# Kernel optimization log

Hardware: AMD Instinct MI355X
Metric: run time of the kernel (lower is better)

The kernel has to match this reference:

```python
import jax, jax.numpy as jnp
import numpy as np

N_NODES = 50000
N_EDGES = 800000
D_FEAT = 64
UNITS = 64


def setup_inputs() -> dict:
    key = jax.random.key(0)
    k1, k2, k3, k4, k5 = jax.random.split(key, 5)
    embeddings = jax.random.normal(k1, (N_NODES, D_FEAT), dtype=jnp.float32)
    edge_src = jax.random.randint(k2, (N_EDGES,), 0, N_NODES, dtype=jnp.int32)
    edge_dst = jax.random.randint(k3, (N_EDGES,), 0, N_NODES, dtype=jnp.int32)
    # normalized-adjacency-like positive weights
    edge_w = jax.random.uniform(k4, (N_EDGES,), dtype=jnp.float32)
    # keras 'truncated_normal' initializer default stddev=0.05 (approx w/ normal)
    kernel = jax.random.normal(k5, (D_FEAT, UNITS), dtype=jnp.float32) * 0.05
    return {"embeddings": embeddings, "edge_src": edge_src,
            "edge_dst": edge_dst, "edge_w": edge_w, "kernel": kernel}


def reference(embeddings, edge_src, edge_dst, edge_w, kernel):
    # SpMM: agg[i] = sum_{e: dst(e)=i} w_e * embeddings[src(e)]
    msgs = embeddings[edge_src] * edge_w[:, None]            # [E, D]
    agg = jax.ops.segment_sum(msgs, edge_dst,
                              num_segments=embeddings.shape[0])  # [N, D]
    # dense GEMM + relu (use_bias=False)
    return jax.nn.relu(agg @ kernel)                          # [N, units]
```

## Files before the change

### kernel.cpp

```cpp
#include <hip/hip_runtime.h>
#include <hip/hip_bf16.h>

#define D    64
#define CH   4096
#define BKT  32
#define PASS 1024

__global__ __launch_bounds__(256) void gemm_part(
    const float* __restrict__ emb,
    const float* __restrict__ W,
    __hip_bfloat16* __restrict__ Zb,
    const int*   __restrict__ dst,
    int*         __restrict__ histG,
    ushort*      __restrict__ lrank,
    int N, int E, int NB, int gemmTiles)
{
    __shared__ int smem[4096];

    if ((int)blockIdx.x >= gemmTiles) {
        const int c  = (int)blockIdx.x - gemmTiles;
        const int t  = threadIdx.x;
        for (int b = t; b < NB; b += 256) smem[b] = 0;
        __syncthreads();
        const int e0 = c * CH;
#pragma unroll
        for (int i = 0; i < 16; ++i) {
            int e = e0 + i * 256 + t;
            if (e < E) {
                int b = dst[e] / BKT;
                lrank[e] = (ushort)atomicAdd(&smem[b], 1);
            }
        }
        __syncthreads();
        for (int b = t; b < NB; b += 256)
            histG[(size_t)c * NB + b] = smem[b];
        return;
    }

    const int lane = threadIdx.x & 63;
    const int wave = threadIdx.x >> 6;

    float wcol[D];
#pragma unroll
    for (int k = 0; k < D; ++k) wcol[k] = W[k * D + lane];

    float* At = (float*)smem;
    const int row0 = blockIdx.x * 64;

    for (int i = threadIdx.x; i < 1024; i += 256) {
        int r  = i >> 4;
        int gr = row0 + r;
        float4 v;
        if (gr < N) v = reinterpret_cast<const float4*>(emb)[(size_t)gr * 16 + (i & 15)];
        else        v = float4{0.f, 0.f, 0.f, 0.f};
        reinterpret_cast<float4*>(At)[i] = v;
    }
    __syncthreads();

    for (int rr = 0; rr < 16; ++rr) {
        int r  = wave * 16 + rr;
        int gr = row0 + r;
        if (gr >= N) break;
        const float4* arow = reinterpret_cast<const float4*>(At + r * D);
        float acc = 0.f;
#pragma unroll
        for (int k4 = 0; k4 < 16; ++k4) {
            float4 a = arow[k4];
            acc = fmaf(a.x, wcol[4 * k4 + 0], acc);
            acc = fmaf(a.y, wcol[4 * k4 + 1], acc);
            acc = fmaf(a.z, wcol[4 * k4 + 2], acc);
            acc = fmaf(a.w, wcol[4 * k4 + 3], acc);
        }
        Zb[(size_t)gr * D + lane] = __float2bfloat16(acc);
    }
}

__global__ __launch_bounds__(256) void scan_hist(
    const int* __restrict__ histG, int* __restrict__ offsets,
    int* __restrict__ partials, int NB, int NC, int M)
{
    __shared__ int sh[256];
    const int t    = threadIdx.x;
    const int base = blockIdx.x * 4096 + t * 16;

    int v[16], ps[16];
    int b = base / NC, c = base - b * NC;
#pragma unroll
    for (int k = 0; k < 16; ++k) {
        int m = base + k;
        v[k] = (m < M) ? histG[(size_t)c * NB + b] : 0;
        if (++c == NC) { c = 0; ++b; }
    }
    int s = 0;
#pragma unroll
    for (int k = 0; k < 16; ++k) { ps[k] = s; s += v[k]; }
    sh[t] = s;
    __syncthreads();
    for (int off = 1; off < 256; off <<= 1) {
        int x = (t >= off) ? sh[t - off] : 0;
        __syncthreads();
        sh[t] += x;
        __syncthreads();
    }
    const int excl = sh[t] - s;
#pragma unroll
    for (int k = 0; k < 4; ++k) {
        int4 o;
        o.x = excl + ps[4*k+0]; o.y = excl + ps[4*k+1];
        o.z = excl + ps[4*k+2]; o.w = excl + ps[4*k+3];
        reinterpret_cast<int4*>(offsets + base)[k] = o;
    }
    if (t == 255) partials[blockIdx.x] = sh[255];
}

__device__ __forceinline__ void scan_partials_lds256(
    const int* __restrict__ partials, int nb, int* sp)
{
    const int t    = threadIdx.x;
    const int orig = (t < nb) ? partials[t] : 0;
    sp[t] = orig;
    __syncthreads();
    for (int off = 1; off < 256; off <<= 1) {
        int x = (t >= off) ? sp[t - off] : 0;
        __syncthreads();
        sp[t] += x;
        __syncthreads();
    }
    int incl = sp[t];
    __syncthreads();
    sp[t] = incl - orig;
    __syncthreads();
}

__global__ __launch_bounds__(256) void scatter_bkt(
    const int*    __restrict__ src,
    const int*    __restrict__ dst,
    const float*  __restrict__ w,
    const ushort* __restrict__ lrank,
    const int*    __restrict__ histG,
    const int*    __restrict__ offsets,
    const int*    __restrict__ partials,
    int2*         __restrict__ csr,
    int E, int NB, int NC, int nb2)
{
    __shared__ int2   rec[CH];
    __shared__ ushort bidv[CH];
    __shared__ int    delta[1568];
    __shared__ int    sh[256];
    __shared__ int    sp[256];
    scan_partials_lds256(partials, nb2, sp);

    const int t  = threadIdx.x;
    const int c  = blockIdx.x;
    const int e0 = c * CH;
    const int cnt = min(CH, E - e0);

    int hv[7], hps[7];
    const int hbase = t * 7;
#pragma unroll
    for (int k = 0; k < 7; ++k) {
        int b = hbase + k;
        hv[k] = (b < NB) ? histG[(size_t)c * NB + b] : 0;
    }
    int s = 0;
#pragma unroll
    for (int k = 0; k < 7; ++k) { hps[k] = s; s += hv[k]; }
    sh[t] = s;
    __syncthreads();
    for (int off = 1; off < 256; off <<= 1) {
        int x = (t >= off) ? sh[t - off] : 0;
        __syncthreads();
        sh[t] += x;
        __syncthreads();
    }
    const int hexcl = sh[t] - s;
#pragma unroll
    for (int k = 0; k < 7; ++k) {
        int b = hbase + k;
        if (b < NB) delta[b] = hexcl + hps[k];
    }
    __syncthreads();

#pragma unroll
    for (int i = 0; i < 16; ++i) {
        int e = e0 + i * 256 + t;
        if (e < E) {
            int d  = dst[e];
            int b  = d / BKT;
            int lp = delta[b] + lrank[e];
            rec[lp]  = make_int2(src[e] | ((d & (BKT - 1)) << 16), __float_as_int(w[e]));
            bidv[lp] = (ushort)b;
        }
    }
    __syncthreads();

#pragma unroll
    for (int k = 0; k < 7; ++k) {
        int b = hbase + k;
        if (b < NB) {
            int m = b * NC + c;
            delta[b] = offsets[m] + sp[m >> 12] - delta[b];
        }
    }
    __syncthreads();

    for (int j = t; j < cnt; j += 256)
        csr[j + delta[bidv[j]]] = rec[j];
}

__global__ __launch_bounds__(256) void aggregate(
    const __hip_bfloat16* __restrict__ Zb,
    const int2* __restrict__ csr,
    const int*  __restrict__ offsets,
    const int*  __restrict__ partials,
    float*      __restrict__ out,
    int N, int E, int NB, int NC, int nb2)
{
    __shared__ int2 srec[PASS];
    __shared__ int  hist[BKT];
    __shared__ int  nbase[BKT + 1];
    __shared__ int  sp[256];
    scan_partials_lds256(partials, nb2, sp);

    const int t = threadIdx.x;
    const int b = blockIdx.x;

    const int m0 = b * NC;
    const int bStart = offsets[m0] + sp[m0 >> 12];
    int bEnd;
    if (b + 1 < NB) { int m1 = (b + 1) * NC; bEnd = offsets[m1] + sp[m1 >> 12]; }
    else            bEnd = E;

    const int wv   = t >> 6;
    const int lane = t & 63;
    const int slot = lane >> 3;
    const int q    = lane & 7;

    const int4* Zq = reinterpret_cast<const int4*>(Zb);

    float4 alo[8], ahi[8];
#pragma unroll
    for (int r = 0; r < 8; ++r) { alo[r] = float4{0,0,0,0}; ahi[r] = float4{0,0,0,0}; }

    for (int cur = bStart; cur < bEnd; cur += PASS) {
        const int cnt = min(PASS, bEnd - cur);

        if (t < BKT) hist[t] = 0;
        __syncthreads();

        int2 myrec[4]; int mypos[4];
#pragma unroll
        for (int k = 0; k < 4; ++k) {
            int j = k * 256 + t;
            if (j < cnt) {
                int2 r2 = csr[cur + j];
                myrec[k] = r2;
                mypos[k] = atomicAdd(&hist[(r2.x >> 16) & (BKT - 1)], 1);
            }
        }
        __syncthreads();

        if (t < BKT) {
            int v = hist[t];
            int x = v;
            for (int off = 1; off < BKT; off <<= 1) {
                int y = __shfl_up(x, off, 64);
                if (t >= off) x += y;
            }
            nbase[t] = x - v;
            if (t == BKT - 1) nbase[BKT] = x;
        }
        __syncthreads();

#pragma unroll
        for (int k = 0; k < 4; ++k) {
            int j = k * 256 + t;
            if (j < cnt)
                srec[nbase[(myrec[k].x >> 16) & (BKT - 1)] + mypos[k]] = myrec[k];
        }
        __syncthreads();

        for (int r = 0; r < 8; ++r) {
            const int nl = wv * 8 + r;
            const int je = nbase[nl + 1];
            for (int j = nbase[nl] + slot; j < je; j += 8) {
                int2  e  = srec[j];
                float ww = __int_as_float(e.y);
                int   sn = e.x & 0xFFFF;
                int4  zz = Zq[(size_t)sn * 8 + q];
                alo[r].x = fmaf(ww, __uint_as_float((unsigned)zz.x << 16),          alo[r].x);
                alo[r].y = fmaf(ww, __uint_as_float((unsigned)zz.x & 0xFFFF0000u),  alo[r].y);
                alo[r].z = fmaf(ww, __uint_as_float((unsigned)zz.y << 16),          alo[r].z);
                alo[r].w = fmaf(ww, __uint_as_float((unsigned)zz.y & 0xFFFF0000u),  alo[r].w);
                ahi[r].x = fmaf(ww, __uint_as_float((unsigned)zz.z << 16),          ahi[r].x);
                ahi[r].y = fmaf(ww, __uint_as_float((unsigned)zz.z & 0xFFFF0000u),  ahi[r].y);
                ahi[r].z = fmaf(ww, __uint_as_float((unsigned)zz.w << 16),          ahi[r].z);
                ahi[r].w = fmaf(ww, __uint_as_float((unsigned)zz.w & 0xFFFF0000u),  ahi[r].w);
            }
        }
        __syncthreads();
    }

    const int node0 = b * BKT + wv * 8;
#pragma unroll
    for (int r = 0; r < 8; ++r) {
        float4 lo = alo[r], hi = ahi[r];
#pragma unroll
        for (int off = 32; off >= 8; off >>= 1) {
            lo.x += __shfl_down(lo.x, off, 64);
            lo.y += __shfl_down(lo.y, off, 64);
            lo.z += __shfl_down(lo.z, off, 64);
            lo.w += __shfl_down(lo.w, off, 64);
            hi.x += __shfl_down(hi.x, off, 64);
            hi.y += __shfl_down(hi.y, off, 64);
            hi.z += __shfl_down(hi.z, off, 64);
            hi.w += __shfl_down(hi.w, off, 64);
        }
        int node = node0 + r;
        if (lane < 8 && node < N) {
            float4 o0, o1;
            o0.x = fmaxf(lo.x, 0.f); o0.y = fmaxf(lo.y, 0.f);
            o0.z = fmaxf(lo.z, 0.f); o0.w = fmaxf(lo.w, 0.f);
            o1.x = fmaxf(hi.x, 0.f); o1.y = fmaxf(hi.y, 0.f);
            o1.z = fmaxf(hi.z, 0.f); o1.w = fmaxf(hi.w, 0.f);
            float4* orow = reinterpret_cast<float4*>(out) + (size_t)node * 16 + lane * 2;
            orow[0] = o0;
            orow[1] = o1;
        }
    }
}

extern "C" void kernel_launch(void* const* d_in, const int* in_sizes, int n_in,
                              void* d_out, int out_size, void* d_ws, size_t ws_size,
                              hipStream_t stream)
{
    const float* emb  = (const float*)d_in[0];
    const int*   esrc = (const int*)  d_in[1];
    const int*   edst = (const int*)  d_in[2];
    const float* ew   = (const float*)d_in[3];
    const float* W    = (const float*)d_in[4];
    float*       out  = (float*)d_out;

    const int N  = in_sizes[0] / D;
    const int E  = in_sizes[1];

    const int NB  = (N + BKT - 1) / BKT;
    const int NC  = (E + CH - 1) / CH;
    const int M   = NB * NC;
    const int nb2 = (M + 4095) / 4096;
    const int Mpad = nb2 * 4096;

    char* p = (char*)d_ws;
    __hip_bfloat16* Zb = (__hip_bfloat16*)p;  p += (size_t)N * D * 2;
    int*    histG   = (int*)p;                p += (size_t)Mpad * 4;
    int*    offsets = (int*)p;                p += (size_t)Mpad * 4;
    int*    partials= (int*)p;                p += 256 * 4;
    ushort* lrank   = (ushort*)p;             p += (size_t)((E + 7) & ~7) * 2;
    int2*   csr     = (int2*)p;

    const int gemmTiles = (N + 63) / 64;
    gemm_part<<<gemmTiles + NC, 256, 0, stream>>>(
        emb, W, Zb, edst, histG, lrank, N, E, NB, gemmTiles);

    scan_hist<<<nb2, 256, 0, stream>>>(histG, offsets, partials, NB, NC, M);

    scatter_bkt<<<NC, 256, 0, stream>>>(
        esrc, edst, ew, lrank, histG, offsets, partials, csr, E, NB, NC, nb2);

    aggregate<<<NB, 256, 0, stream>>>(
        Zb, csr, offsets, partials, out, N, E, NB, NC, nb2);
}
```

Baseline: 147.4 us.

## Fuse all four stages into one cooperative persistent kernel with grid syncs

Replaces the four separate launches (GEMM+histogram, scan, scatter, aggregate) with one persistent cooperative kernel that uses grid-wide syncs between phases. The histogram is now stored bucket-major so the scan reads it contiguously. The scatter phase recomputes each chunk's local histogram rather than reading it back. This is meant to remove launch gaps and redundant per-block partial scans, at the cost of grid.sync overhead, a grid capped at occupancy-based persistent size, and a 48KB shared buffer that may limit occupancy.

```diff
diff --git a/kernel.cpp b/kernel.cpp
--- a/kernel.cpp
+++ b/kernel.cpp
@@ -1,331 +1,296 @@
 #include <hip/hip_runtime.h>
+#include <hip/hip_cooperative_groups.h>
 #include <hip/hip_bf16.h>
+
+namespace cg = cooperative_groups;
 
 #define D    64
 #define CH   4096
 #define BKT  32
 #define PASS 1024
-
-__global__ __launch_bounds__(256) void gemm_part(
+#define SU   2048
+
+__global__ __launch_bounds__(256, 2) void fused(
     const float* __restrict__ emb,
     const float* __restrict__ W,
+    const int*   __restrict__ esrc,
+    const int*   __restrict__ edst,
+    const float* __restrict__ ew,
+    float*       __restrict__ out,
     __hip_bfloat16* __restrict__ Zb,
-    const int*   __restrict__ dst,
-    int*         __restrict__ histG,
-    ushort*      __restrict__ lrank,
-    int N, int E, int NB, int gemmTiles)
+    int*    __restrict__ histG,
+    int*    __restrict__ offsets,
+    int*    __restrict__ partials,
+    ushort* __restrict__ lrank,
+    int2*   __restrict__ csr,
+    int N, int E, int NB, int NC, int M, int units, int gemmTiles)
 {
-    __shared__ int smem[4096];
-
-    if ((int)blockIdx.x >= gemmTiles) {
-        const int c  = (int)blockIdx.x - gemmTiles;
-        const int t  = threadIdx.x;
-        for (int b = t; b < NB; b += 256) smem[b] = 0;
+    __shared__ __align__(16) char smem[49152];
+    cg::grid_group grid = cg::this_grid();
+    const int t = threadIdx.x;
+    const int G = gridDim.x;
+
+    for (int it = blockIdx.x; it < gemmTiles + NC; it += G) {
         __syncthreads();
-        const int e0 = c * CH;
-#pragma unroll
-        for (int i = 0; i < 16; ++i) {
-            int e = e0 + i * 256 + t;
-            if (e < E) {
-                int b = dst[e] / BKT;
-                lrank[e] = (ushort)atomicAdd(&smem[b], 1);
-            }
-        }
+        if (it < gemmTiles) {
+            float* At = (float*)smem;
+            const int lane = t & 63, wave = t >> 6;
+            float wcol[D];
+#pragma unroll
+            for (int k = 0; k < D; ++k) wcol[k] = W[k * D + lane];
+            const int row0 = it * 64;
+            for (int i = t; i < 1024; i += 256) {
+                int r = i >> 4, gr = row0 + r;
+                float4 v = (gr < N)
+                    ? reinterpret_cast<const float4*>(emb)[(size_t)gr * 16 + (i & 15)]
+                    : float4{0.f, 0.f, 0.f, 0.f};
+                reinterpret_cast<float4*>(At)[i] = v;
+            }
+            __syncthreads();
+            for (int rr = 0; rr < 16; ++rr) {
+                int r = wave * 16 + rr, gr = row0 + r;
+                if (gr >= N) break;
+                const float4* arow = reinterpret_cast<const float4*>(At + r * D);
+                float acc = 0.f;
+#pragma unroll
+                for (int k4 = 0; k4 < 16; ++k4) {
+                    float4 a = arow[k4];
+                    acc = fmaf(a.x, wcol[4 * k4 + 0], acc);
+                    acc = fmaf(a.y, wcol[4 * k4 + 1], acc);
+                    acc = fmaf(a.z, wcol[4 * k4 + 2], acc);
+                    acc = fmaf(a.w, wcol[4 * k4 + 3], acc);
+                }
+                Zb[(size_t)gr * D + lane] = __float2bfloat16(acc);
+            }
+        } else {
+            const int c = it - gemmTiles;
+            int* hist = (int*)smem;
+            for (int b = t; b < NB; b += 256) hist[b] = 0;
+            __syncthreads();
+            const int e0 = c * CH;
+#pragma unroll
+            for (int i = 0; i < 16; ++i) {
+                int e = e0 + i * 256 + t;
+                if (e < E)
+                    lrank[e] = (ushort)atomicAdd(&hist[edst[e] >> 5], 1);
+            }
+            __syncthreads();
+            for (int b = t; b < NB; b += 256)
+                histG[(size_t)b * NC + c] = hist[b];
+        }
+    }
+    grid.sync();
+
+    for (int u = blockIdx.x; u < units; u += G) {
         __syncthreads();
-        for (int b = t; b < NB; b += 256)
-            histG[(size_t)c * NB + b] = smem[b];
-        return;
-    }
-
-    const int lane = threadIdx.x & 63;
-    const int wave = threadIdx.x >> 6;
-
-    float wcol[D];
-#pragma unroll
-    for (int k = 0; k < D; ++k) wcol[k] = W[k * D + lane];
-
-    float* At = (float*)smem;
-    const int row0 = blockIdx.x * 64;
-
-    for (int i = threadIdx.x; i < 1024; i += 256) {
-        int r  = i >> 4;
-        int gr = row0 + r;
-        float4 v;
-        if (gr < N) v = reinterpret_cast<const float4*>(emb)[(size_t)gr * 16 + (i & 15)];
-        else        v = float4{0.f, 0.f, 0.f, 0.f};
-        reinterpret_cast<float4*>(At)[i] = v;
-    }
-    __syncthreads();
-
-    for (int rr = 0; rr < 16; ++rr) {
-        int r  = wave * 16 + rr;
-        int gr = row0 + r;
-        if (gr >= N) break;
-        const float4* arow = reinterpret_cast<const float4*>(At + r * D);
-        float acc = 0.f;
-#pragma unroll
-        for (int k4 = 0; k4 < 16; ++k4) {
-            float4 a = arow[k4];
-            acc = fmaf(a.x, wcol[4 * k4 + 0], acc);
-            acc = fmaf(a.y, wcol[4 * k4 + 1], acc);
-            acc = fmaf(a.z, wcol[4 * k4 + 2], acc);
-            acc = fmaf(a.w, wcol[4 * k4 + 3], acc);
-        }
-        Zb[(size_t)gr * D + lane] = __float2bfloat16(acc);
-    }
-}
-
-__global__ __launch_bounds__(256) void scan_hist(
-    const int* __restrict__ histG, int* __restrict__ offsets,
-    int* __restrict__ partials, int NB, int NC, int M)
-{
-    __shared__ int sh[256];
-    const int t    = threadIdx.x;
-    const int base = blockIdx.x * 4096 + t * 16;
-
-    int v[16], ps[16];
-    int b = base / NC, c = base - b * NC;
-#pragma unroll
-    for (int k = 0; k < 16; ++k) {
-        int m = base + k;
-        v[k] = (m < M) ? histG[(size_t)c * NB + b] : 0;
-        if (++c == NC) { c = 0; ++b; }
-    }
-    int s = 0;
-#pragma unroll
-    for (int k = 0; k < 16; ++k) { ps[k] = s; s += v[k]; }
-    sh[t] = s;
-    __syncthreads();
-    for (int off = 1; off < 256; off <<= 1) {
-        int x = (t >= off) ? sh[t - off] : 0;
+        int* sh = (int*)smem;
+        const int base = u * SU + t * 8;
+        int v[8], ps[8];
+#pragma unroll
+        for (int k = 0; k < 8; ++k) {
+            int m = base + k;
+            v[k] = (m < M) ? histG[m] : 0;
+        }
+        int s = 0;
+#pragma unroll
+        for (int k = 0; k < 8; ++k) { ps[k] = s; s += v[k]; }
+        sh[t] = s;
         __syncthreads();
-        sh[t] += x;
+        for (int off = 1; off < 256; off <<= 1) {
+            int x = (t >= off) ? sh[t - off] : 0;
+            __syncthreads();
+            sh[t] += x;
+            __syncthreads();
+        }
+        const int excl = sh[t] - s;
+#pragma unroll
+        for (int k = 0; k < 8; ++k)
+            offsets[base + k] = excl + ps[k];
+        if (t == 255) partials[u] = sh[255];
+    }
+    grid.sync();
+
+    if (blockIdx.x == 0) {
+        int* sh = (int*)smem;
+        int orig = (t < units) ? partials[t] : 0;
+        sh[t] = orig;
         __syncthreads();
-    }
-    const int excl = sh[t] - s;
-#pragma unroll
-    for (int k = 0; k < 4; ++k) {
-        int4 o;
-        o.x = excl + ps[4*k+0]; o.y = excl + ps[4*k+1];
-        o.z = excl + ps[4*k+2]; o.w = excl + ps[4*k+3];
-        reinterpret_cast<int4*>(offsets + base)[k] = o;
-    }
-    if (t == 255) partials[blockIdx.x] = sh[255];
-}
-
-__device__ __forceinline__ void scan_partials_lds256(
-    const int* __restrict__ partials, int nb, int* sp)
-{
-    const int t    = threadIdx.x;
-    const int orig = (t < nb) ? partials[t] : 0;
-    sp[t] = orig;
-    __syncthreads();
-    for (int off = 1; off < 256; off <<= 1) {
-        int x = (t >= off) ? sp[t - off] : 0;
-        __syncthreads();
-        sp[t] += x;
-        __syncthreads();
-    }
-    int incl = sp[t];
-    __syncthreads();
-    sp[t] = incl - orig;
-    __syncthreads();
-}
-
-__global__ __launch_bounds__(256) void scatter_bkt(
-    const int*    __restrict__ src,
-    const int*    __restrict__ dst,
-    const float*  __restrict__ w,
-    const ushort* __restrict__ lrank,
-    const int*    __restrict__ histG,
-    const int*    __restrict__ offsets,
-    const int*    __restrict__ partials,
-    int2*         __restrict__ csr,
-    int E, int NB, int NC, int nb2)
-{
-    __shared__ int2   rec[CH];
-    __shared__ ushort bidv[CH];
-    __shared__ int    delta[1568];
-    __shared__ int    sh[256];
-    __shared__ int    sp[256];
-    scan_partials_lds256(partials, nb2, sp);
-
-    const int t  = threadIdx.x;
-    const int c  = blockIdx.x;
-    const int e0 = c * CH;
-    const int cnt = min(CH, E - e0);
-
-    int hv[7], hps[7];
-    const int hbase = t * 7;
-#pragma unroll
-    for (int k = 0; k < 7; ++k) {
-        int b = hbase + k;
-        hv[k] = (b < NB) ? histG[(size_t)c * NB + b] : 0;
-    }
-    int s = 0;
-#pragma unroll
-    for (int k = 0; k < 7; ++k) { hps[k] = s; s += hv[k]; }
-    sh[t] = s;
-    __syncthreads();
-    for (int off = 1; off < 256; off <<= 1) {
-        int x = (t >= off) ? sh[t - off] : 0;
-        __syncthreads();
-        sh[t] += x;
-        __syncthreads();
-    }
-    const int hexcl = sh[t] - s;
-#pragma unroll
-    for (int k = 0; k < 7; ++k) {
-        int b = hbase + k;
-        if (b < NB) delta[b] = hexcl + hps[k];
-    }
-    __syncthreads();
-
-#pragma unroll
-    for (int i = 0; i < 16; ++i) {
-        int e = e0 + i * 256 + t;
-        if (e < E) {
-            int d  = dst[e];
-            int b  = d / BKT;
-            int lp = delta[b] + lrank[e];
-            rec[lp]  = make_int2(src[e] | ((d & (BKT - 1)) << 16), __float_as_int(w[e]));
-            bidv[lp] = (ushort)b;
-        }
-    }
-    __syncthreads();
-
-#pragma unroll
-    for (int k = 0; k < 7; ++k) {
-        int b = hbase + k;
-        if (b < NB) {
-            int m = b * NC + c;
-            delta[b] = offsets[m] + sp[m >> 12] - delta[b];
-        }
-    }
-    __syncthreads();
-
-    for (int j = t; j < cnt; j += 256)
-        csr[j + delta[bidv[j]]] = rec[j];
-}
-
-__global__ __launch_bounds__(256) void aggregate(
-    const __hip_bfloat16* __restrict__ Zb,
-    const int2* __restrict__ csr,
-    const int*  __restrict__ offsets,
-    const int*  __restrict__ partials,
-    float*      __restrict__ out,
-    int N, int E, int NB, int NC, int nb2)
-{
-    __shared__ int2 srec[PASS];
-    __shared__ int  hist[BKT];
-    __shared__ int  nbase[BKT + 1];
-    __shared__ int  sp[256];
-    scan_partials_lds256(partials, nb2, sp);
-
-    const int t = threadIdx.x;
-    const int b = blockIdx.x;
-
-    const int m0 = b * NC;
-    const int bStart = offsets[m0] + sp[m0 >> 12];
-    int bEnd;
-    if (b + 1 < NB) { int m1 = (b + 1) * NC; bEnd = offsets[m1] + sp[m1 >> 12]; }
-    else            bEnd = E;
-
-    const int wv   = t >> 6;
-    const int lane = t & 63;
-    const int slot = lane >> 3;
-    const int q    = lane & 7;
-
-    const int4* Zq = reinterpret_cast<const int4*>(Zb);
-
-    float4 alo[8], ahi[8];
-#pragma unroll
-    for (int r = 0; r < 8; ++r) { alo[r] = float4{0,0,0,0}; ahi[r] = float4{0,0,0,0}; }
-
-    for (int cur = bStart; cur < bEnd; cur += PASS) {
-        const int cnt = min(PASS, bEnd - cur);
-
-        if (t < BKT) hist[t] = 0;
-        __syncthreads();
-
-        int2 myrec[4]; int mypos[4];
-#pragma unroll
-        for (int k = 0; k < 4; ++k) {
-            int j = k * 256 + t;
-            if (j < cnt) {
-                int2 r2 = csr[cur + j];
-                myrec[k] = r2;
-                mypos[k] = atomicAdd(&hist[(r2.x >> 16) & (BKT - 1)], 1);
-            }
-        }
-        __syncthreads();
-
-        if (t < BKT) {
-            int v = hist[t];
-            int x = v;
-            for (int off = 1; off < BKT; off <<= 1) {
-                int y = __shfl_up(x, off, 64);
-                if (t >= off) x += y;
-            }
-            nbase[t] = x - v;
-            if (t == BKT - 1) nbase[BKT] = x;
-        }
-        __syncthreads();
-
-#pragma unroll
-        for (int k = 0; k < 4; ++k) {
-            int j = k * 256 + t;
-            if (j < cnt)
-                srec[nbase[(myrec[k].x >> 16) & (BKT - 1)] + mypos[k]] = myrec[k];
-        }
-        __syncthreads();
-
-        for (int r = 0; r < 8; ++r) {
-            const int nl = wv * 8 + r;
-            const int je = nbase[nl + 1];
-            for (int j = nbase[nl] + slot; j < je; j += 8) {
-                int2  e  = srec[j];
-                float ww = __int_as_float(e.y);
-                int   sn = e.x & 0xFFFF;
-                int4  zz = Zq[(size_t)sn * 8 + q];
-                alo[r].x = fmaf(ww, __uint_as_float((unsigned)zz.x << 16),          alo[r].x);
-                alo[r].y = fmaf(ww, __uint_as_float((unsigned)zz.x & 0xFFFF0000u),  alo[r].y);
-                alo[r].z = fmaf(ww, __uint_as_float((unsigned)zz.y << 16),          alo[r].z);
-                alo[r].w = fmaf(ww, __uint_as_float((unsigned)zz.y & 0xFFFF0000u),  alo[r].w);
-                ahi[r].x = fmaf(ww, __uint_as_float((unsigned)zz.z << 16),          ahi[r].x);
-                ahi[r].y = fmaf(ww, __uint_as_float((unsigned)zz.z & 0xFFFF0000u),  ahi[r].y);
-                ahi[r].z = fmaf(ww, __uint_as_float((unsigned)zz.w << 16),          ahi[r].z);
-                ahi[r].w = fmaf(ww, __uint_as_float((unsigned)zz.w & 0xFFFF0000u),  ahi[r].w);
-            }
-        }
-        __syncthreads();
-    }
-
-    const int node0 = b * BKT + wv * 8;
-#pragma unroll
-    for (int r = 0; r < 8; ++r) {
-        float4 lo = alo[r], hi = ahi[r];
-#pragma unroll
-        for (int off = 32; off >= 8; off >>= 1) {
-            lo.x += __shfl_down(lo.x, off, 64);
-            lo.y += __shfl_down(lo.y, off, 64);
-            lo.z += __shfl_down(lo.z, off, 64);
-            lo.w += __shfl_down(lo.w, off, 64);
-            hi.x += __shfl_down(hi.x, off, 64);
-            hi.y += __shfl_down(hi.y, off, 64);
-            hi.z += __shfl_down(hi.z, off, 64);
-            hi.w += __shfl_down(hi.w, off, 64);
-        }
-        int node = node0 + r;
-        if (lane < 8 && node < N) {
-            float4 o0, o1;
-            o0.x = fmaxf(lo.x, 0.f); o0.y = fmaxf(lo.y, 0.f);
-            o0.z = fmaxf(lo.z, 0.f); o0.w = fmaxf(lo.w, 0.f);
-            o1.x = fmaxf(hi.x, 0.f); o1.y = fmaxf(hi.y, 0.f);
-            o1.z = fmaxf(hi.z, 0.f); o1.w = fmaxf(hi.w, 0.f);
-            float4* orow = reinterpret_cast<float4*>(out) + (size_t)node * 16 + lane * 2;
-            orow[0] = o0;
-            orow[1] = o1;
+        for (int off = 1; off < 256; off <<= 1) {
+            int x = (t >= off) ? sh[t - off] : 0;
+            __syncthreads();
+            sh[t] += x;
+            __syncthreads();
+        }
+        if (t < units) partials[t] = sh[t] - orig;
+    }
+    grid.sync();
+
+    {
+        int2*   rec  = (int2*)smem;
+        ushort* bidv = (ushort*)(smem + 32768);
+        int*    lcnt = (int*)(smem + 40960);
+        int*    sh   = (int*)(smem + 47232);
+        for (int c = blockIdx.x; c < NC; c += G) {
+            __syncthreads();
+            const int e0  = c * CH;
+            const int cnt = min(CH, E - e0);
+            for (int b = t; b < NB; b += 256) lcnt[b] = 0;
+            __syncthreads();
+#pragma unroll
+            for (int i = 0; i < 16; ++i) {
+                int e = e0 + i * 256 + t;
+                if (e < E) atomicAdd(&lcnt[edst[e] >> 5], 1);
+            }
+            __syncthreads();
+            int hv[7], ps[7];
+            const int hbase = t * 7;
+#pragma unroll
+            for (int k = 0; k < 7; ++k) {
+                int b = hbase + k;
+                hv[k] = (b < NB) ? lcnt[b] : 0;
+            }
+            int s = 0;
+#pragma unroll
+            for (int k = 0; k < 7; ++k) { ps[k] = s; s += hv[k]; }
+            sh[t] = s;
+            __syncthreads();
+            for (int off = 1; off < 256; off <<= 1) {
+                int x = (t >= off) ? sh[t - off] : 0;
+                __syncthreads();
+                sh[t] += x;
+                __syncthreads();
+            }
+            const int hexcl = sh[t] - s;
+#pragma unroll
+            for (int k = 0; k < 7; ++k) {
+                int b = hbase + k;
+                if (b < NB) lcnt[b] = hexcl + ps[k];
+            }
+            __syncthreads();
+#pragma unroll
+            for (int i = 0; i < 16; ++i) {
+                int e = e0 + i * 256 + t;
+                if (e < E) {
+                    int d  = edst[e];
+                    int b  = d >> 5;
+                    int lp = lcnt[b] + lrank[e];
+                    rec[lp]  = make_int2(esrc[e] | ((d & 31) << 16), __float_as_int(ew[e]));
+                    bidv[lp] = (ushort)b;
+                }
+            }
+            __syncthreads();
+#pragma unroll
+            for (int k = 0; k < 7; ++k) {
+                int b = hbase + k;
+                if (b < NB) {
+                    int m = b * NC + c;
+                    lcnt[b] = offsets[m] + partials[m >> 11] - lcnt[b];
+                }
+            }
+            __syncthreads();
+            for (int j = t; j < cnt; j += 256)
+                csr[j + lcnt[bidv[j]]] = rec[j];
+        }
+    }
+    grid.sync();
+
+    {
+        int2* srec  = (int2*)smem;
+        int*  hist  = (int*)(smem + 8192);
+        int*  nbase = (int*)(smem + 8192 + 128);
+        const int wv = t >> 6, lane = t & 63, slot = lane >> 3, q = lane & 7;
+        const int4* Zq = reinterpret_cast<const int4*>(Zb);
+
+        for (int b = blockIdx.x; b < NB; b += G) {
+            __syncthreads();
+            const int m0 = b * NC, m1 = m0 + NC;
+            const int bStart = offsets[m0] + partials[m0 >> 11];
+            const int bEnd   = offsets[m1] + partials[m1 >> 11];
+
+            float4 alo[8], ahi[8];
+#pragma unroll
+            for (int r = 0; r < 8; ++r) { alo[r] = float4{0,0,0,0}; ahi[r] = float4{0,0,0,0}; }
+
+            for (int cur = bStart; cur < bEnd; cur += PASS) {
+                const int cnt = min(PASS, bEnd - cur);
+                if (t < BKT) hist[t] = 0;
+                __syncthreads();
+                int2 myrec[4]; int mypos[4];
+#pragma unroll
+                for (int k = 0; k < 4; ++k) {
+                    int j = k * 256 + t;
+                    if (j < cnt) {
+                        int2 r2 = csr[cur + j];
+                        myrec[k] = r2;
+                        mypos[k] = atomicAdd(&hist[(r2.x >> 16) & (BKT - 1)], 1);
+                    }
+                }
+                __syncthreads();
+                if (t < BKT) {
+                    int v = hist[t], x = v;
+                    for (int off = 1; off < BKT; off <<= 1) {
+                        int y = __shfl_up(x, off, 64);
+                        if (t >= off) x += y;
+                    }
+                    nbase[t] = x - v;
+                    if (t == BKT - 1) nbase[BKT] = x;
+                }
+                __syncthreads();
+#pragma unroll
+                for (int k = 0; k < 4; ++k) {
+                    int j = k * 256 + t;
+                    if (j < cnt)
+                        srec[nbase[(myrec[k].x >> 16) & (BKT - 1)] + mypos[k]] = myrec[k];
+                }
+                __syncthreads();
+                for (int r = 0; r < 8; ++r) {
+                    const int nl = wv * 8 + r;
+                    const int je = nbase[nl + 1];
+                    for (int j = nbase[nl] + slot; j < je; j += 8) {
+                        int2  e  = srec[j];
+                        float ww = __int_as_float(e.y);
+                        int   sn = e.x & 0xFFFF;
+                        int4  zz = Zq[(size_t)sn * 8 + q];
+                        alo[r].x = fmaf(ww, __uint_as_float((unsigned)zz.x << 16),         alo[r].x);
+                        alo[r].y = fmaf(ww, __uint_as_float((unsigned)zz.x & 0xFFFF0000u), alo[r].y);
+                        alo[r].z = fmaf(ww, __uint_as_float((unsigned)zz.y << 16),         alo[r].z);
+                        alo[r].w = fmaf(ww, __uint_as_float((unsigned)zz.y & 0xFFFF0000u), alo[r].w);
+                        ahi[r].x = fmaf(ww, __uint_as_float((unsigned)zz.z << 16),         ahi[r].x);
+                        ahi[r].y = fmaf(ww, __uint_as_float((unsigned)zz.z & 0xFFFF0000u), ahi[r].y);
+                        ahi[r].z = fmaf(ww, __uint_as_float((unsigned)zz.w << 16),         ahi[r].z);
+                        ahi[r].w = fmaf(ww, __uint_as_float((unsigned)zz.w & 0xFFFF0000u), ahi[r].w);
+                    }
+                }
+                __syncthreads();
+            }
+
+            const int node0 = b * BKT + wv * 8;
+#pragma unroll
+            for (int r = 0; r < 8; ++r) {
+                float4 lo = alo[r], hi = ahi[r];
+#pragma unroll
+                for (int off = 32; off >= 8; off >>= 1) {
+                    lo.x += __shfl_down(lo.x, off, 64);
+                    lo.y += __shfl_down(lo.y, off, 64);
+                    lo.z += __shfl_down(lo.z, off, 64);
+                    lo.w += __shfl_down(lo.w, off, 64);
+                    hi.x += __shfl_down(hi.x, off, 64);
+                    hi.y += __shfl_down(hi.y, off, 64);
+                    hi.z += __shfl_down(hi.z, off, 64);
+                    hi.w += __shfl_down(hi.w, off, 64);
+                }
+                int node = node0 + r;
+                if (lane < 8 && node < N) {
+                    float4 o0, o1;
+                    o0.x = fmaxf(lo.x, 0.f); o0.y = fmaxf(lo.y, 0.f);
+                    o0.z = fmaxf(lo.z, 0.f); o0.w = fmaxf(lo.w, 0.f);
+                    o1.x = fmaxf(hi.x, 0.f); o1.y = fmaxf(hi.y, 0.f);
+                    o1.z = fmaxf(hi.z, 0.f); o1.w = fmaxf(hi.w, 0.f);
+                    float4* orow = reinterpret_cast<float4*>(out) + (size_t)node * 16 + lane * 2;
+                    orow[0] = o0;
+                    orow[1] = o1;
+                }
+            }
         }
     }
 }
@@ -344,29 +309,32 @@
     const int N  = in_sizes[0] / D;
     const int E  = in_sizes[1];
 
-    const int NB  = (N + BKT - 1) / BKT;
-    const int NC  = (E + CH - 1) / CH;
-    const int M   = NB * NC;
-    const int nb2 = (M + 4095) / 4096;
-    const int Mpad = nb2 * 4096;
+    const int NB    = (N + BKT - 1) / BKT;
+    const int NC    = (E + CH - 1) / CH;
+    const int M     = NB * NC;
+    const int units = (M + SU - 1) / SU;
+    const int Mpad  = units * SU;
+    const int gemmTiles = (N + 63) / 64;
 
     char* p = (char*)d_ws;
     __hip_bfloat16* Zb = (__hip_bfloat16*)p;  p += (size_t)N * D * 2;
-    int*    histG   = (int*)p;                p += (size_t)Mpad * 4;
-    int*    offsets = (int*)p;                p += (size_t)Mpad * 4;
-    int*    partials= (int*)p;                p += 256 * 4;
-    ushort* lrank   = (ushort*)p;             p += (size_t)((E + 7) & ~7) * 2;
-    int2*   csr     = (int2*)p;
-
-    const int gemmTiles = (N + 63) / 64;
-    gemm_part<<<gemmTiles + NC, 256, 0, stream>>>(
-        emb, W, Zb, edst, histG, lrank, N, E, NB, gemmTiles);
-
-    scan_hist<<<nb2, 256, 0, stream>>>(histG, offsets, partials, NB, NC, M);
-
-    scatter_bkt<<<NC, 256, 0, stream>>>(
-        esrc, edst, ew, lrank, histG, offsets, partials, csr, E, NB, NC, nb2);
-
-    aggregate<<<NB, 256, 0, stream>>>(
-        Zb, csr, offsets, partials, out, N, E, NB, NC, nb2);
+    int*    histG    = (int*)p;               p += (size_t)Mpad * 4;
+    int*    offsets  = (int*)p;               p += (size_t)Mpad * 4;
+    int*    partials = (int*)p;               p += 256 * 4;
+    ushort* lrank    = (ushort*)p;            p += (size_t)((E + 7) & ~7) * 2;
+    int2*   csr      = (int2*)p;
+
+    int bpc = 0;
+    if (hipOccupancyMaxActiveBlocksPerMultiprocessor(&bpc, fused, 256, 0) != hipSuccess
+        || bpc < 1)
+        bpc = 2;
+    int grid = bpc * 256;
+    if (grid > 2048) grid = 2048;
+
+    int n = N, e = E, nb = NB, nc = NC, m = M, un = units, gt = gemmTiles;
+    void* args[] = { (void*)&emb, (void*)&W, (void*)&esrc, (void*)&edst, (void*)&ew,
+                     (void*)&out, (void*)&Zb, (void*)&histG, (void*)&offsets,
+                     (void*)&partials, (void*)&lrank, (void*)&csr,
+                     &n, &e, &nb, &nc, &m, &un, &gt };
+    hipLaunchCooperativeKernel(fused, dim3(grid), dim3(256), args, 0, stream);
 }
```

Measured after the change: 364.0 us. 147% more time.

## Drop lrank buffer, transpose histogram layout, vectorize edge loads, prefetch aggregate gathers

Applied to the files above, without the earlier changes.

The histogram pass no longer stores a per-edge local rank. Scatter now recomputes the ranks with LDS atomics while loading src/dst/w as int4/float4, and packs the bucket id into the record's upper bits, which removes the lrank global write and read plus the bidv array. The histogram is written bucket-major so the scan reads it contiguously, with 2048-element scan units. The aggregate inner loop issues the first three gathers up front for more memory parallelism. The cost is that in-bucket edge order becomes nondeterministic and the packed-bit scheme is limited to node counts that fit in 16 bits.

```diff
diff --git a/kernel.cpp b/kernel.cpp
--- a/kernel.cpp
+++ b/kernel.cpp
@@ -5,6 +5,7 @@
 #define CH   4096
 #define BKT  32
 #define PASS 1024
+#define SU   2048
 
 __global__ __launch_bounds__(256) void gemm_part(
     const float* __restrict__ emb,
@@ -12,28 +13,32 @@
     __hip_bfloat16* __restrict__ Zb,
     const int*   __restrict__ dst,
     int*         __restrict__ histG,
-    ushort*      __restrict__ lrank,
-    int N, int E, int NB, int gemmTiles)
+    int N, int E, int NB, int NC, int gemmTiles)
 {
     __shared__ int smem[4096];
 
     if ((int)blockIdx.x >= gemmTiles) {
-        const int c  = (int)blockIdx.x - gemmTiles;
-        const int t  = threadIdx.x;
+        const int c   = (int)blockIdx.x - gemmTiles;
+        const int t   = threadIdx.x;
+        const int e0  = c * CH;
+        const int cnt = min(CH, E - e0);
         for (int b = t; b < NB; b += 256) smem[b] = 0;
         __syncthreads();
-        const int e0 = c * CH;
-#pragma unroll
-        for (int i = 0; i < 16; ++i) {
-            int e = e0 + i * 256 + t;
-            if (e < E) {
-                int b = dst[e] / BKT;
-                lrank[e] = (ushort)atomicAdd(&smem[b], 1);
+        const int4* d4p = reinterpret_cast<const int4*>(dst + e0);
+#pragma unroll
+        for (int i = 0; i < 4; ++i) {
+            int g = i * 256 + t;
+            if (g * 4 < cnt) {
+                int4 d4 = d4p[g];
+                atomicAdd(&smem[d4.x >> 5], 1);
+                atomicAdd(&smem[d4.y >> 5], 1);
+                atomicAdd(&smem[d4.z >> 5], 1);
+                atomicAdd(&smem[d4.w >> 5], 1);
             }
         }
         __syncthreads();
         for (int b = t; b < NB; b += 256)
-            histG[(size_t)c * NB + b] = smem[b];
+            histG[(size_t)b * NC + c] = smem[b];
         return;
     }
 
@@ -48,18 +53,16 @@
     const int row0 = blockIdx.x * 64;
 
     for (int i = threadIdx.x; i < 1024; i += 256) {
-        int r  = i >> 4;
-        int gr = row0 + r;
-        float4 v;
-        if (gr < N) v = reinterpret_cast<const float4*>(emb)[(size_t)gr * 16 + (i & 15)];
-        else        v = float4{0.f, 0.f, 0.f, 0.f};
+        int r = i >> 4, gr = row0 + r;
+        float4 v = (gr < N)
+            ? reinterpret_cast<const float4*>(emb)[(size_t)gr * 16 + (i & 15)]
+            : float4{0.f, 0.f, 0.f, 0.f};
         reinterpret_cast<float4*>(At)[i] = v;
     }
     __syncthreads();
 
     for (int rr = 0; rr < 16; ++rr) {
-        int r  = wave * 16 + rr;
-        int gr = row0 + r;
+        int r = wave * 16 + rr, gr = row0 + r;
         if (gr >= N) break;
         const float4* arow = reinterpret_cast<const float4*>(At + r * D);
         float acc = 0.f;
@@ -77,23 +80,21 @@
 
 __global__ __launch_bounds__(256) void scan_hist(
     const int* __restrict__ histG, int* __restrict__ offsets,
-    int* __restrict__ partials, int NB, int NC, int M)
+    int* __restrict__ partials, int M)
 {
     __shared__ int sh[256];
     const int t    = threadIdx.x;
-    const int base = blockIdx.x * 4096 + t * 16;
-
-    int v[16], ps[16];
-    int b = base / NC, c = base - b * NC;
-#pragma unroll
-    for (int k = 0; k < 16; ++k) {
+    const int base = blockIdx.x * SU + t * 8;
+
+    int v[8], ps[8];
+#pragma unroll
+    for (int k = 0; k < 8; ++k) {
         int m = base + k;
-        v[k] = (m < M) ? histG[(size_t)c * NB + b] : 0;
-        if (++c == NC) { c = 0; ++b; }
+        v[k] = (m < M) ? histG[m] : 0;
     }
     int s = 0;
 #pragma unroll
-    for (int k = 0; k < 16; ++k) { ps[k] = s; s += v[k]; }
+    for (int k = 0; k < 8; ++k) { ps[k] = s; s += v[k]; }
     sh[t] = s;
     __syncthreads();
     for (int off = 1; off < 256; off <<= 1) {
@@ -104,20 +105,16 @@
     }
     const int excl = sh[t] - s;
 #pragma unroll
-    for (int k = 0; k < 4; ++k) {
-        int4 o;
-        o.x = excl + ps[4*k+0]; o.y = excl + ps[4*k+1];
-        o.z = excl + ps[4*k+2]; o.w = excl + ps[4*k+3];
-        reinterpret_cast<int4*>(offsets + base)[k] = o;
-    }
+    for (int k = 0; k < 8; ++k)
+        offsets[base + k] = excl + ps[k];
     if (t == 255) partials[blockIdx.x] = sh[255];
 }
 
 __device__ __forceinline__ void scan_partials_lds256(
-    const int* __restrict__ partials, int nb, int* sp)
+    const int* __restrict__ partials, int nu, int* sp)
 {
     const int t    = threadIdx.x;
-    const int orig = (t < nb) ? partials[t] : 0;
+    const int orig = (t < nu) ? partials[t] : 0;
     sp[t] = orig;
     __syncthreads();
     for (int off = 1; off < 256; off <<= 1) {
@@ -133,38 +130,65 @@
 }
 
 __global__ __launch_bounds__(256) void scatter_bkt(
-    const int*    __restrict__ src,
-    const int*    __restrict__ dst,
-    const float*  __restrict__ w,
-    const ushort* __restrict__ lrank,
-    const int*    __restrict__ histG,
-    const int*    __restrict__ offsets,
-    const int*    __restrict__ partials,
-    int2*         __restrict__ csr,
-    int E, int NB, int NC, int nb2)
-{
-    __shared__ int2   rec[CH];
-    __shared__ ushort bidv[CH];
-    __shared__ int    delta[1568];
-    __shared__ int    sh[256];
-    __shared__ int    sp[256];
-    scan_partials_lds256(partials, nb2, sp);
-
-    const int t  = threadIdx.x;
-    const int c  = blockIdx.x;
-    const int e0 = c * CH;
+    const int*   __restrict__ src,
+    const int*   __restrict__ dst,
+    const float* __restrict__ w,
+    const int*   __restrict__ offsets,
+    const int*   __restrict__ partials,
+    int2*        __restrict__ csr,
+    int E, int NB, int NC, int units)
+{
+    __shared__ int2 rec[CH];
+    __shared__ int  lcnt[1568];
+    __shared__ int  sh[256];
+    __shared__ int  sp[256];
+    scan_partials_lds256(partials, units, sp);
+
+    const int t   = threadIdx.x;
+    const int c   = blockIdx.x;
+    const int e0  = c * CH;
     const int cnt = min(CH, E - e0);
 
-    int hv[7], hps[7];
+    for (int b = t; b < NB; b += 256) lcnt[b] = 0;
+    __syncthreads();
+
+    int2 myrec[16]; int mypos[16];
+    const int4*   s4p = reinterpret_cast<const int4*>(src + e0);
+    const int4*   d4p = reinterpret_cast<const int4*>(dst + e0);
+    const float4* w4p = reinterpret_cast<const float4*>(w + e0);
+#pragma unroll
+    for (int i = 0; i < 4; ++i) {
+        int g = i * 256 + t;
+        if (g * 4 < cnt) {
+            int4   s4 = s4p[g];
+            int4   d4 = d4p[g];
+            float4 w4 = w4p[g];
+            int b0 = d4.x >> 5, b1 = d4.y >> 5, b2 = d4.z >> 5, b3 = d4.w >> 5;
+            myrec[4*i+0] = make_int2(s4.x | ((d4.x & 31) << 16) | (b0 << 21), __float_as_int(w4.x));
+            myrec[4*i+1] = make_int2(s4.y | ((d4.y & 31) << 16) | (b1 << 21), __float_as_int(w4.y));
+            myrec[4*i+2] = make_int2(s4.z | ((d4.z & 31) << 16) | (b2 << 21), __float_as_int(w4.z));
+            myrec[4*i+3] = make_int2(s4.w | ((d4.w & 31) << 16) | (b3 << 21), __float_as_int(w4.w));
+            mypos[4*i+0] = atomicAdd(&lcnt[b0], 1);
+            mypos[4*i+1] = atomicAdd(&lcnt[b1], 1);
+            mypos[4*i+2] = atomicAdd(&lcnt[b2], 1);
+            mypos[4*i+3] = atomicAdd(&lcnt[b3], 1);
+        } else {
+#pragma unroll
+            for (int k = 0; k < 4; ++k) mypos[4*i+k] = -1;
+        }
+    }
+    __syncthreads();
+
+    int hv[7], ps[7];
     const int hbase = t * 7;
 #pragma unroll
     for (int k = 0; k < 7; ++k) {
         int b = hbase + k;
-        hv[k] = (b < NB) ? histG[(size_t)c * NB + b] : 0;
+        hv[k] = (b < NB) ? lcnt[b] : 0;
     }
     int s = 0;
 #pragma unroll
-    for (int k = 0; k < 7; ++k) { hps[k] = s; s += hv[k]; }
+    for (int k = 0; k < 7; ++k) { ps[k] = s; s += hv[k]; }
     sh[t] = s;
     __syncthreads();
     for (int off = 1; off < 256; off <<= 1) {
@@ -174,23 +198,18 @@
         __syncthreads();
     }
     const int hexcl = sh[t] - s;
+    __syncthreads();
 #pragma unroll
     for (int k = 0; k < 7; ++k) {
         int b = hbase + k;
-        if (b < NB) delta[b] = hexcl + hps[k];
-    }
-    __syncthreads();
-
-#pragma unroll
-    for (int i = 0; i < 16; ++i) {
-        int e = e0 + i * 256 + t;
-        if (e < E) {
-            int d  = dst[e];
-            int b  = d / BKT;
-            int lp = delta[b] + lrank[e];
-            rec[lp]  = make_int2(src[e] | ((d & (BKT - 1)) << 16), __float_as_int(w[e]));
-            bidv[lp] = (ushort)b;
-        }
+        if (b < NB) lcnt[b] = hexcl + ps[k];
+    }
+    __syncthreads();
+
+#pragma unroll
+    for (int k = 0; k < 16; ++k) {
+        if (mypos[k] >= 0)
+            rec[lcnt[(unsigned)myrec[k].x >> 21] + mypos[k]] = myrec[k];
     }
     __syncthreads();
 
@@ -199,13 +218,15 @@
         int b = hbase + k;
         if (b < NB) {
             int m = b * NC + c;
-            delta[b] = offsets[m] + sp[m >> 12] - delta[b];
-        }
-    }
-    __syncthreads();
-
-    for (int j = t; j < cnt; j += 256)
-        csr[j + delta[bidv[j]]] = rec[j];
+            lcnt[b] = offsets[m] + sp[m >> 11] - lcnt[b];
+        }
+    }
+    __syncthreads();
+
+    for (int j = t; j < cnt; j += 256) {
+        int2 rj = rec[j];
+        csr[j + lcnt[(unsigned)rj.x >> 21]] = rj;
+    }
 }
 
 __global__ __launch_bounds__(256) void aggregate(
@@ -214,37 +235,42 @@
     const int*  __restrict__ offsets,
     const int*  __restrict__ partials,
     float*      __restrict__ out,
-    int N, int E, int NB, int NC, int nb2)
+    int N, int NB, int NC, int units)
 {
     __shared__ int2 srec[PASS];
     __shared__ int  hist[BKT];
     __shared__ int  nbase[BKT + 1];
     __shared__ int  sp[256];
-    scan_partials_lds256(partials, nb2, sp);
+    scan_partials_lds256(partials, units, sp);
 
     const int t = threadIdx.x;
     const int b = blockIdx.x;
 
-    const int m0 = b * NC;
-    const int bStart = offsets[m0] + sp[m0 >> 12];
-    int bEnd;
-    if (b + 1 < NB) { int m1 = (b + 1) * NC; bEnd = offsets[m1] + sp[m1 >> 12]; }
-    else            bEnd = E;
-
-    const int wv   = t >> 6;
-    const int lane = t & 63;
-    const int slot = lane >> 3;
-    const int q    = lane & 7;
-
+    const int m0 = b * NC, m1 = m0 + NC;
+    const int bStart = offsets[m0] + sp[m0 >> 11];
+    const int bEnd   = offsets[m1] + sp[m1 >> 11];
+
+    const int wv = t >> 6, lane = t & 63, slot = lane >> 3, q = lane & 7;
     const int4* Zq = reinterpret_cast<const int4*>(Zb);
 
     float4 alo[8], ahi[8];
 #pragma unroll
     for (int r = 0; r < 8; ++r) { alo[r] = float4{0,0,0,0}; ahi[r] = float4{0,0,0,0}; }
+
+#define FMA8(LO, HI, WW, ZZ)                                                     \
+    do {                                                                         \
+        (LO).x = fmaf((WW), __uint_as_float((unsigned)(ZZ).x << 16),        (LO).x); \
+        (LO).y = fmaf((WW), __uint_as_float((unsigned)(ZZ).x & 0xFFFF0000u),(LO).y); \
+        (LO).z = fmaf((WW), __uint_as_float((unsigned)(ZZ).y << 16),        (LO).z); \
+        (LO).w = fmaf((WW), __uint_as_float((unsigned)(ZZ).y & 0xFFFF0000u),(LO).w); \
+        (HI).x = fmaf((WW), __uint_as_float((unsigned)(ZZ).z << 16),        (HI).x); \
+        (HI).y = fmaf((WW), __uint_as_float((unsigned)(ZZ).z & 0xFFFF0000u),(HI).y); \
+        (HI).z = fmaf((WW), __uint_as_float((unsigned)(ZZ).w << 16),        (HI).z); \
+        (HI).w = fmaf((WW), __uint_as_float((unsigned)(ZZ).w & 0xFFFF0000u),(HI).w); \
+    } while (0)
 
     for (int cur = bStart; cur < bEnd; cur += PASS) {
         const int cnt = min(PASS, bEnd - cur);
-
         if (t < BKT) hist[t] = 0;
         __syncthreads();
 
@@ -256,13 +282,12 @@
                 int2 r2 = csr[cur + j];
                 myrec[k] = r2;
                 mypos[k] = atomicAdd(&hist[(r2.x >> 16) & (BKT - 1)], 1);
-            }
+            } else mypos[k] = -1;
         }
         __syncthreads();
 
         if (t < BKT) {
-            int v = hist[t];
-            int x = v;
+            int v = hist[t], x = v;
             for (int off = 1; off < BKT; off <<= 1) {
                 int y = __shfl_up(x, off, 64);
                 if (t >= off) x += y;
@@ -274,28 +299,31 @@
 
 #pragma unroll
         for (int k = 0; k < 4; ++k) {
-            int j = k * 256 + t;
-            if (j < cnt)
+            if (mypos[k] >= 0)
                 srec[nbase[(myrec[k].x >> 16) & (BKT - 1)] + mypos[k]] = myrec[k];
         }
         __syncthreads();
 
         for (int r = 0; r < 8; ++r) {
             const int nl = wv * 8 + r;
+            const int jb = nbase[nl] + slot;
             const int je = nbase[nl + 1];
-            for (int j = nbase[nl] + slot; j < je; j += 8) {
-                int2  e  = srec[j];
-                float ww = __int_as_float(e.y);
-                int   sn = e.x & 0xFFFF;
-                int4  zz = Zq[(size_t)sn * 8 + q];
-                alo[r].x = fmaf(ww, __uint_as_float((unsigned)zz.x << 16),          alo[r].x);
-                alo[r].y = fmaf(ww, __uint_as_float((unsigned)zz.x & 0xFFFF0000u),  alo[r].y);
-                alo[r].z = fmaf(ww, __uint_as_float((unsigned)zz.y << 16),          alo[r].z);
-                alo[r].w = fmaf(ww, __uint_as_float((unsigned)zz.y & 0xFFFF0000u),  alo[r].w);
-                ahi[r].x = fmaf(ww, __uint_as_float((unsigned)zz.z << 16),          ahi[r].x);
-                ahi[r].y = fmaf(ww, __uint_as_float((unsigned)zz.z & 0xFFFF0000u),  ahi[r].y);
-                ahi[r].z = fmaf(ww, __uint_as_float((unsigned)zz.w << 16),          ahi[r].z);
-                ahi[r].w = fmaf(ww, __uint_as_float((unsigned)zz.w & 0xFFFF0000u),  ahi[r].w);
+            const int j1 = jb + 8, j2 = jb + 16;
+            int2 e0 = make_int2(0, 0), e1 = make_int2(0, 0), e2 = make_int2(0, 0);
+            if (jb < je) e0 = srec[jb];
+            if (j1 < je) e1 = srec[j1];
+            if (j2 < je) e2 = srec[j2];
+            int4 z0 = make_int4(0,0,0,0), z1 = make_int4(0,0,0,0), z2 = make_int4(0,0,0,0);
+            if (jb < je) z0 = Zq[(size_t)(e0.x & 0xFFFF) * 8 + q];
+            if (j1 < je) z1 = Zq[(size_t)(e1.x & 0xFFFF) * 8 + q];
+            if (j2 < je) z2 = Zq[(size_t)(e2.x & 0xFFFF) * 8 + q];
+            FMA8(alo[r], ahi[r], __int_as_float(e0.y), z0);
+            FMA8(alo[r], ahi[r], __int_as_float(e1.y), z1);
+            FMA8(alo[r], ahi[r], __int_as_float(e2.y), z2);
+            for (int j = j2 + 8; j < je; j += 8) {
+                int2 e = srec[j];
+                int4 zz = Zq[(size_t)(e.x & 0xFFFF) * 8 + q];
+                FMA8(alo[r], ahi[r], __int_as_float(e.y), zz);
             }
         }
         __syncthreads();
@@ -328,6 +356,7 @@
             orow[1] = o1;
         }
     }
+#undef FMA8
 }
 
 extern "C" void kernel_launch(void* const* d_in, const int* in_sizes, int n_in,
@@ -341,32 +370,31 @@
     const float* W    = (const float*)d_in[4];
     float*       out  = (float*)d_out;
 
-    const int N  = in_sizes[0] / D;
-    const int E  = in_sizes[1];
-
-    const int NB  = (N + BKT - 1) / BKT;
-    const int NC  = (E + CH - 1) / CH;
-    const int M   = NB * NC;
-    const int nb2 = (M + 4095) / 4096;
-    const int Mpad = nb2 * 4096;
+    const int N = in_sizes[0] / D;
+    const int E = in_sizes[1];
+
+    const int NB    = (N + BKT - 1) / BKT;
+    const int NC    = (E + CH - 1) / CH;
+    const int M     = NB * NC;
+    const int units = (M + SU - 1) / SU;
+    const int Mpad  = units * SU;
+    const int gemmTiles = (N + 63) / 64;
 
     char* p = (char*)d_ws;
     __hip_bfloat16* Zb = (__hip_bfloat16*)p;  p += (size_t)N * D * 2;
-    int*    histG   = (int*)p;                p += (size_t)Mpad * 4;
-    int*    offsets = (int*)p;                p += (size_t)Mpad * 4;
-    int*    partials= (int*)p;                p += 256 * 4;
-    ushort* lrank   = (ushort*)p;             p += (size_t)((E + 7) & ~7) * 2;
-    int2*   csr     = (int2*)p;
-
-    const int gemmTiles = (N + 63) / 64;
+    int*  histG    = (int*)p;                 p += (size_t)Mpad * 4;
+    int*  offsets  = (int*)p;                 p += (size_t)Mpad * 4;
+    int*  partials = (int*)p;                 p += 256 * 4;
+    int2* csr      = (int2*)p;
+
     gemm_part<<<gemmTiles + NC, 256, 0, stream>>>(
-        emb, W, Zb, edst, histG, lrank, N, E, NB, gemmTiles);
-
-    scan_hist<<<nb2, 256, 0, stream>>>(histG, offsets, partials, NB, NC, M);
+        emb, W, Zb, edst, histG, N, E, NB, NC, gemmTiles);
+
+    scan_hist<<<units, 256, 0, stream>>>(histG, offsets, partials, M);
 
     scatter_bkt<<<NC, 256, 0, stream>>>(
-        esrc, edst, ew, lrank, histG, offsets, partials, csr, E, NB, NC, nb2);
+        esrc, edst, ew, offsets, partials, csr, E, NB, NC, units);
 
     aggregate<<<NB, 256, 0, stream>>>(
-        Zb, csr, offsets, partials, out, N, E, NB, NC, nb2);
-}
+        Zb, csr, offsets, partials, out, N, NB, NC, units);
+}
```

New measurement: 139.3 us. 5.5% less time.
